# Kernel tuning notes

Hardware: AMD Instinct MI355X
Metric: run time of the kernel (lower is better)

The kernel has to match this reference:

```python
import jax, jax.numpy as jnp
import numpy as np

KLD_SCALE = 10.0
COMMIT_COST = 0.25


def setup_inputs() -> dict:
    key = jax.random.key(0)
    k1, k2, k3, k4 = jax.random.split(key, 4)
    B, C, T = 32, 512, 4096
    D, K = 128, 1024
    z = jax.random.normal(k1, (B, C, T), dtype=jnp.float32)
    proj_w = jax.random.normal(k2, (D, C), dtype=jnp.float32) * (1.0 / np.sqrt(C))
    proj_b = jax.random.normal(k3, (D,), dtype=jnp.float32) * 0.01
    embed_w = jax.random.normal(k4, (K, D), dtype=jnp.float32)
    return {"z": z, "proj_w": proj_w, "proj_b": proj_b, "embed_w": embed_w}


def reference(z, proj_w, proj_b, embed_w):
    B, C, T = z.shape
    D = proj_w.shape[0]
    # 1x1 Conv1d == per-timestep linear: [B,C,T] x [D,C] -> [B,T,D]
    z_e = jnp.einsum('bct,dc->btd', z, proj_w) + proj_b
    flat = z_e.reshape(-1, D)  # [B*T, D]
    # squared euclidean distances to codebook: [B*T, K]
    dist = (jnp.sum(flat * flat, axis=1, keepdims=True)
            - 2.0 * (flat @ embed_w.T)
            + jnp.sum(embed_w * embed_w, axis=1)[None, :])
    ind = jnp.argmin(dist, axis=1).reshape(B, T)  # == argmax(-dist)
    z_q = embed_w[ind]  # [B,T,D] codebook gather
    sg = jax.lax.stop_gradient
    diff = KLD_SCALE * (COMMIT_COST * jnp.mean((sg(z_q) - z_e) ** 2)
                        + jnp.mean((z_q - sg(z_e)) ** 2))
    z_q_ste = z_e + sg(z_q - z_e)  # straight-through estimator
    z_q_out = jnp.transpose(z_q_ste, (0, 2, 1))  # [B,D,T]
    return z_q_out, diff, ind
```

## Files before the change

kernel.cpp:

```cpp
#include <hip/hip_runtime.h>

#define B_N 32
#define C_N 512
#define T_N 4096
#define D_N 128
#define K_N 1024
#define N_N (B_N * T_N)

typedef _Float16 f16x8 __attribute__((ext_vector_type(8)));
typedef float    f32x4 __attribute__((ext_vector_type(4)));

#define ZSWZ_OFF 0
#define ESWZ_OFF 67108864
#define ENS_OFF  67895296
#define WSWZ_OFF 68431872
#define PART_OFF 68694016

#define GLL(g, s) __builtin_amdgcn_global_load_lds( \
    (const __attribute__((address_space(1))) unsigned int*)(g), \
    (__attribute__((address_space(3))) unsigned int*)(s), 16, 0, 0)

__global__ __launch_bounds__(128) void k_eprep(const float* __restrict__ E,
                                               _Float16* __restrict__ eswz,
                                               float* __restrict__ ens) {
  __shared__ float s2[2];
  const int code = blockIdx.x, d = threadIdx.x;
  const float e  = E[(size_t)code * D_N + d];
  const float es = e * 64.f;
  const _Float16 eh = (_Float16)es;
  const _Float16 el = (_Float16)(es - (float)eh);

  float sq = es * es;
  #pragma unroll
  for (int off = 32; off > 0; off >>= 1) sq += __shfl_down(sq, off);
  if ((d & 63) == 0) s2[d >> 6] = sq;
  __syncthreads();
  if (d == 0) ens[code] = s2[0] + s2[1];

  const int kt = code >> 7, mi = (code >> 4) & 7, lrow = code & 15;
  const int lk = (d >> 3) & 3, i = d & 7, cb = d >> 5;
  const size_t tile = (size_t)kt * 12;
  #define PUT(c, v) eswz[(((tile + (c)) * 512 + mi * 64 + lk * 16 + lrow) << 3) + i] = (v)
  PUT(cb, eh);
  PUT(4 + cb, el);
  PUT(8 + cb, eh);
  #undef PUT
}

__global__ __launch_bounds__(256) void k_wprep(const float* __restrict__ W,
                                               _Float16* __restrict__ wswz) {
  const int e = blockIdx.x * 256 + threadIdx.x;
  const int d = e >> 9, c = e & 511;
  const float x = W[d * C_N + c] * 8.f;
  const _Float16 h  = (_Float16)x;
  const _Float16 lo = (_Float16)(x - (float)h);
  const int kc = c >> 5, gg = (c >> 3) & 3, j = c & 7;
  const int nf = d >> 4, ll = gg * 16 + (d & 15);
  const size_t base = (size_t)kc * 8192 + ((size_t)nf * 64 + ll) * 8 + j;
  wswz[base]        = h;
  wswz[base + 4096] = lo;
}

__global__ __launch_bounds__(256, 2) void k_projm(const float* __restrict__ z,
                                                  const _Float16* __restrict__ wswz,
                                                  const float* __restrict__ bias,
                                                  f16x8* __restrict__ zswz) {
  __shared__ __align__(16) char lds[65536];

  const int tid = threadIdx.x;
  const int l   = tid & 63, w = tid >> 6;
  const int g   = l >> 4, li = l & 15;
  const int b   = blockIdx.y, t0 = blockIdx.x * 128;
  const float* zb = z + (size_t)b * C_N * T_N + t0;

  float bs[8];
  #pragma unroll
  for (int nf = 0; nf < 8; ++nf) bs[nf] = bias[nf * 16 + li] * 64.f;

  f32x4 acc[2][8];
  #pragma unroll
  for (int mi = 0; mi < 2; ++mi)
    #pragma unroll
    for (int nf = 0; nf < 8; ++nf) acc[mi][nf] = (f32x4)0.f;

  auto stage = [&](int kc, int buf) {
    char* zdst = lds + buf * 16384;
    char* wdst = lds + 32768 + buf * 16384;
    #pragma unroll
    for (int s = 0; s < 4; ++s) {
      const int q = w * 4 + s;
      const unsigned v = q * 64 + l;
      const unsigned u = v ^ (((v >> 8) & 1) << 2);
      GLL((const char*)zb +
              ((size_t)(kc * 32 + (u >> 5)) * T_N + (size_t)(u & 31) * 4) * 4,
          zdst + q * 1024);
      GLL((const char*)wswz + (size_t)kc * 16384 + q * 1024 + l * 16,
          wdst + q * 1024);
    }
  };

  stage(0, 0);
  __syncthreads();

  int buf = 0;
  for (int kc = 0; kc < 16; ++kc) {
    if (kc + 1 < 16) stage(kc + 1, buf ^ 1);

    const float* zl = (const float*)(lds + buf * 16384);
    const f16x8* wb = (const f16x8*)(lds + 32768 + buf * 16384);

    f16x8 ah[2], al[2];
    #pragma unroll
    for (int mi = 0; mi < 2; ++mi) {
      const int mt = w * 2 + mi;
      const int a0 = (g * 1024 + mt * 16 + li) ^ ((g & 1) << 4);
      #pragma unroll
      for (int j = 0; j < 8; ++j) {
        const float x = zl[a0 + j * 128] * 8.f;
        const _Float16 h = (_Float16)x;
        ah[mi][j] = h;
        al[mi][j] = (_Float16)(x - (float)h);
      }
    }
    f16x8 bh[8], bl[8];
    #pragma unroll
    for (int nf = 0; nf < 8; ++nf) {
      bh[nf] = wb[nf * 64 + l];
      bl[nf] = wb[512 + nf * 64 + l];
    }
    #pragma unroll
    for (int mi = 0; mi < 2; ++mi)
      #pragma unroll
      for (int nf = 0; nf < 8; ++nf) {
        acc[mi][nf] = __builtin_amdgcn_mfma_f32_16x16x32_f16(ah[mi], bh[nf], acc[mi][nf], 0, 0, 0);
        acc[mi][nf] = __builtin_amdgcn_mfma_f32_16x16x32_f16(al[mi], bh[nf], acc[mi][nf], 0, 0, 0);
        acc[mi][nf] = __builtin_amdgcn_mfma_f32_16x16x32_f16(ah[mi], bl[nf], acc[mi][nf], 0, 0, 0);
      }
    __syncthreads();
    buf ^= 1;
  }

  unsigned* cs = (unsigned*)lds;
  const int n0 = b * T_N + t0;
  for (int p = 0; p < 2; ++p) {
    #pragma unroll
    for (int mi = 0; mi < 2; ++mi) {
      const int trow = (w * 2 + mi) * 16 + g * 4;
      #pragma unroll
      for (int nfl = 0; nfl < 4; ++nfl) {
        const int nf = p * 4 + nfl;
        #pragma unroll
        for (int r = 0; r < 4; ++r) {
          const float x = acc[mi][nf][r] + bs[nf];
          const _Float16 h  = (_Float16)x;
          const _Float16 lo = (_Float16)(x - (float)h);
          cs[(trow + r) * 68 + nfl * 16 + li] =
              (unsigned)__builtin_bit_cast(unsigned short, h) |
              ((unsigned)__builtin_bit_cast(unsigned short, lo) << 16);
        }
      }
    }
    __syncthreads();
    #pragma unroll
    for (int i = 0; i < 4; ++i) {
      const int u = i * 256 + tid;
      const int t = u & 127, dc = u >> 7;
      f16x8 vh, vl;
      #pragma unroll
      for (int e = 0; e < 8; ++e) {
        const unsigned vv = cs[t * 68 + dc * 8 + e];
        vh[e] = __builtin_bit_cast(_Float16, (unsigned short)(vv & 0xffff));
        vl[e] = __builtin_bit_cast(_Float16, (unsigned short)(vv >> 16));
      }
      const int n = n0 + t;
      const int cu = p * 2 + (dc >> 2), lk = dc & 3;
      const size_t idx = ((size_t)(n >> 4) * 8 + cu) * 64 + lk * 16 + (n & 15);
      zswz[idx]       = vh;
      zswz[idx + 256] = vl;
    }
    __syncthreads();
  }
}

template<int NF0>
__device__ __forceinline__ float gather_reg(int wc, int l, const int* skf,
                                            const float* E, float* ob,
                                            const f16x8 (&bfr)[8][4]) {
  float psum = 0.f;
  #pragma unroll
  for (int nl = 0; nl < 2; ++nl) {
    constexpr int NFA[2] = {NF0, NF0 + 1};
    const int nf = NFA[nl];
    const int r = wc * 64 + nf * 16 + (l & 15);
    const int k = skf[r];
    const float* Er = E + (size_t)k * D_N;
    #pragma unroll
    for (int cu = 0; cu < 4; ++cu) {
      const int d0 = cu * 32 + (l >> 4) * 8;
      const float4 e0 = *(const float4*)(Er + d0);
      const float4 e1 = *(const float4*)(Er + d0 + 4);
      const float ev[8] = {e0.x, e0.y, e0.z, e0.w, e1.x, e1.y, e1.z, e1.w};
      const f16x8 hi = bfr[cu][nf];
      const f16x8 lo = bfr[cu + 4][nf];
      #pragma unroll
      for (int j = 0; j < 8; ++j) {
        const float ze = ((float)hi[j] + (float)lo[j]) * 0.015625f;
        const float df = ev[j] - ze;
        psum += df * df;
        ob[(size_t)(d0 + j) * T_N + r] = ev[j];
      }
    }
  }
  return psum;
}

__global__ __launch_bounds__(256, 2) void k_argmin5(const f16x8* __restrict__ zswz,
                                                    const f16x8* __restrict__ eswz,
                                                    const float* __restrict__ ens,
                                                    const float* __restrict__ E,
                                                    float* __restrict__ out,
                                                    float* __restrict__ indf,
                                                    float* __restrict__ part) {
  __shared__ __align__(16) char sbuf[65536];
  __shared__ float sdl[256];
  __shared__ int   skl[256];
  __shared__ int   skf[128];

  const int tid = threadIdx.x, l = tid & 63, w = tid >> 6;
  const int wr = w >> 1, wc = w & 1;
  const int blk = blockIdx.x;

  const char* zsrc = (const char*)zswz + (size_t)blk * 65536;
  #pragma unroll
  for (int s = 0; s < 16; ++s)
    GLL(zsrc + s * 4096 + tid * 16, sbuf + s * 4096 + w * 1024);
  asm volatile("s_waitcnt vmcnt(0)" ::: "memory");
  __syncthreads();

  f16x8 bfr[8][4];
  #pragma unroll
  for (int cu = 0; cu < 8; ++cu)
    #pragma unroll
    for (int nf = 0; nf < 4; ++nf)
      bfr[cu][nf] =
          *(const f16x8*)(sbuf + (((((wc * 4 + nf) * 8 + cu) * 64) + l) << 4));
  __syncthreads();

  const char* easrc = (const char*)eswz + (size_t)wr * 4096;

  float bestd[4];
  int   bestk[4];
  #pragma unroll
  for (int nf = 0; nf < 4; ++nf) { bestd[nf] = 3.4e38f; bestk[nf] = 0; }

  for (int kt = 0; kt < 8; ++kt) {
    f32x4 acc[4][4];
    #pragma unroll
    for (int mi = 0; mi < 4; ++mi)
      #pragma unroll
      for (int nf = 0; nf < 4; ++nf) acc[mi][nf] = (f32x4)0.f;

    #pragma unroll
    for (int c = 0; c < 12; ++c) {
      constexpr int CUMAP[12] = {0, 1, 2, 3, 0, 1, 2, 3, 4, 5, 6, 7};
      const int cu = CUMAP[c];
      f16x8 afr[4];
      #pragma unroll
      for (int mi = 0; mi < 4; ++mi)
        afr[mi] = *(const f16x8*)(easrc + (size_t)(kt * 12 + c) * 8192 +
                                  ((mi * 64 + l) << 4));
      #pragma unroll
      for (int mi = 0; mi < 4; ++mi)
        #pragma unroll
        for (int nf = 0; nf < 4; ++nf)
          acc[mi][nf] = __builtin_amdgcn_mfma_f32_16x16x32_f16(
              afr[mi], bfr[cu][nf], acc[mi][nf], 0, 0, 0);
    }

    #pragma unroll
    for (int mi = 0; mi < 4; ++mi) {
      const int cbase = kt * 128 + wr * 64 + mi * 16 + ((l >> 4) << 2);
      const float4 e4 = *(const float4*)&ens[cbase];
      const float ev[4] = {e4.x, e4.y, e4.z, e4.w};
      #pragma unroll
      for (int r = 0; r < 4; ++r) {
        const int k = cbase + r;
        #pragma unroll
        for (int nf = 0; nf < 4; ++nf) {
          const float dv = ev[r] - 2.0f * acc[mi][nf][r];
          if (dv < bestd[nf]) { bestd[nf] = dv; bestk[nf] = k; }
        }
      }
    }
  }

  #pragma unroll
  for (int nf = 0; nf < 4; ++nf) {
    float d = bestd[nf]; int k = bestk[nf];
    #pragma unroll
    for (int off = 16; off < 64; off <<= 1) {
      const float od = __shfl_xor(d, off);
      const int   ok = __shfl_xor(k, off);
      if (od < d || (od == d && ok < k)) { d = od; k = ok; }
    }
    if (l < 16) {
      sdl[wr * 128 + wc * 64 + nf * 16 + l] = d;
      skl[wr * 128 + wc * 64 + nf * 16 + l] = k;
    }
  }
  __syncthreads();
  if (tid < 128) {
    float d0 = sdl[tid], d1 = sdl[128 + tid];
    int   k0 = skl[tid], k1 = skl[128 + tid];
    if (d1 < d0 || (d1 == d0 && k1 < k0)) { d0 = d1; k0 = k1; }
    skf[tid] = k0;
    indf[blk * 128 + tid] = (float)k0;
  }
  __syncthreads();

  const int b  = blk >> 5;
  const int t0 = (blk & 31) << 7;
  float* ob = out + (size_t)b * (D_N * T_N) + t0;
  float psum = (wr == 0) ? gather_reg<0>(wc, l, skf, E, ob, bfr)
                         : gather_reg<2>(wc, l, skf, E, ob, bfr);
  #pragma unroll
  for (int off = 32; off > 0; off >>= 1) psum += __shfl_xor(psum, off);
  if (l == 0) part[blk * 4 + w] = psum;
}

__global__ __launch_bounds__(256) void k_diff(const float* __restrict__ part,
                                              float* __restrict__ diff_out) {
  __shared__ double wsd[4];
  const int tid = threadIdx.x;
  double s = 0.0;
  for (int i = tid; i < 4096; i += 256) s += (double)part[i];
  #pragma unroll
  for (int off = 32; off > 0; off >>= 1) s += __shfl_down(s, off);
  if ((tid & 63) == 0) wsd[tid >> 6] = s;
  __syncthreads();
  if (tid == 0) {
    const double tot = wsd[0] + wsd[1] + wsd[2] + wsd[3];
    diff_out[0] = (float)(12.5 * tot / (double)((size_t)N_N * D_N));
  }
}

extern "C" void kernel_launch(void* const* d_in, const int* in_sizes, int n_in,
                              void* d_out, int out_size, void* d_ws, size_t ws_size,
                              hipStream_t stream) {
  const float* z    = (const float*)d_in[0];
  const float* W    = (const float*)d_in[1];
  const float* bias = (const float*)d_in[2];
  const float* E    = (const float*)d_in[3];

  float* out = (float*)d_out;
  float* out_q    = out;
  float* out_diff = out + 16777216;
  float* out_ind  = out + 16777217;

  char* ws = (char*)d_ws;
  f16x8*    zswz = (f16x8*)(ws + ZSWZ_OFF);
  _Float16* eswz = (_Float16*)(ws + ESWZ_OFF);
  float*    ens  = (float*)(ws + ENS_OFF);
  _Float16* wswz = (_Float16*)(ws + WSWZ_OFF);
  float*    part = (float*)(ws + PART_OFF);

  k_eprep<<<K_N, 128, 0, stream>>>(E, eswz, ens);
  k_wprep<<<256, 256, 0, stream>>>(W, wswz);
  k_projm<<<dim3(T_N / 128, B_N), 256, 0, stream>>>(z, wswz, bias, zswz);
  k_argmin5<<<N_N / 128, 256, 0, stream>>>(zswz, (const f16x8*)eswz, ens, E,
                                           out_q, out_ind, part);
  k_diff<<<1, 256, 0, stream>>>(part, out_diff);
}
```

Measured before the change: 251.8 us.

## Halve argmin tile to 64 rows and double-buffer codebook through LDS

The argmin kernel now handles 64 timesteps per block instead of 128, which doubles the grid and halves the B-fragment registers each wave holds. Codebook fragments are no longer read straight from global memory by each wave. They are staged in a double-buffered LDS ring with async global-to-LDS loads, prefetching the next chunk while MFMAs run on the current one. The per-block partial sums are reduced in shared memory to one value per block. In exchange, the codebook is reloaded twice as many times overall and each chunk adds a barrier.

```diff
diff --git a/kernel.cpp b/kernel.cpp
--- a/kernel.cpp
+++ b/kernel.cpp
@@ -182,99 +182,88 @@
   }
 }
 
-template<int NF0>
-__device__ __forceinline__ float gather_reg(int wc, int l, const int* skf,
-                                            const float* E, float* ob,
-                                            const f16x8 (&bfr)[8][4]) {
-  float psum = 0.f;
-  #pragma unroll
-  for (int nl = 0; nl < 2; ++nl) {
-    constexpr int NFA[2] = {NF0, NF0 + 1};
-    const int nf = NFA[nl];
-    const int r = wc * 64 + nf * 16 + (l & 15);
-    const int k = skf[r];
-    const float* Er = E + (size_t)k * D_N;
-    #pragma unroll
-    for (int cu = 0; cu < 4; ++cu) {
-      const int d0 = cu * 32 + (l >> 4) * 8;
-      const float4 e0 = *(const float4*)(Er + d0);
-      const float4 e1 = *(const float4*)(Er + d0 + 4);
-      const float ev[8] = {e0.x, e0.y, e0.z, e0.w, e1.x, e1.y, e1.z, e1.w};
-      const f16x8 hi = bfr[cu][nf];
-      const f16x8 lo = bfr[cu + 4][nf];
-      #pragma unroll
-      for (int j = 0; j < 8; ++j) {
-        const float ze = ((float)hi[j] + (float)lo[j]) * 0.015625f;
-        const float df = ev[j] - ze;
-        psum += df * df;
-        ob[(size_t)(d0 + j) * T_N + r] = ev[j];
-      }
-    }
-  }
-  return psum;
-}
-
-__global__ __launch_bounds__(256, 2) void k_argmin5(const f16x8* __restrict__ zswz,
+__global__ __launch_bounds__(256, 2) void k_argmin6(const f16x8* __restrict__ zswz,
                                                     const f16x8* __restrict__ eswz,
                                                     const float* __restrict__ ens,
                                                     const float* __restrict__ E,
                                                     float* __restrict__ out,
                                                     float* __restrict__ indf,
                                                     float* __restrict__ part) {
-  __shared__ __align__(16) char sbuf[65536];
-  __shared__ float sdl[256];
-  __shared__ int   skl[256];
-  __shared__ int   skf[128];
+  __shared__ __align__(16) char sbuf[32768];
+  __shared__ float sdl[128];
+  __shared__ int   skl[128];
+  __shared__ int   skf[64];
+  __shared__ float wsum[4];
 
   const int tid = threadIdx.x, l = tid & 63, w = tid >> 6;
   const int wr = w >> 1, wc = w & 1;
   const int blk = blockIdx.x;
 
-  const char* zsrc = (const char*)zswz + (size_t)blk * 65536;
-  #pragma unroll
-  for (int s = 0; s < 16; ++s)
+  const char* zsrc = (const char*)zswz + (size_t)blk * 32768;
+  #pragma unroll
+  for (int s = 0; s < 8; ++s)
     GLL(zsrc + s * 4096 + tid * 16, sbuf + s * 4096 + w * 1024);
   asm volatile("s_waitcnt vmcnt(0)" ::: "memory");
   __syncthreads();
 
-  f16x8 bfr[8][4];
+  f16x8 bfr[8][2];
   #pragma unroll
   for (int cu = 0; cu < 8; ++cu)
     #pragma unroll
-    for (int nf = 0; nf < 4; ++nf)
+    for (int nf = 0; nf < 2; ++nf)
       bfr[cu][nf] =
-          *(const f16x8*)(sbuf + (((((wc * 4 + nf) * 8 + cu) * 64) + l) << 4));
-  __syncthreads();
-
-  const char* easrc = (const char*)eswz + (size_t)wr * 4096;
-
-  float bestd[4];
-  int   bestk[4];
-  #pragma unroll
-  for (int nf = 0; nf < 4; ++nf) { bestd[nf] = 3.4e38f; bestk[nf] = 0; }
+          *(const f16x8*)(sbuf + (((((wc * 2 + nf) * 8 + cu) * 64) + l) << 4));
+  __syncthreads();
+
+  const char* easrc = (const char*)eswz;
+  #pragma unroll
+  for (int s = 0; s < 4; ++s)
+    GLL(easrc + s * 4096 + tid * 16, sbuf + s * 4096 + w * 1024);
+
+  float bestd[2];
+  int   bestk[2];
+  #pragma unroll
+  for (int nf = 0; nf < 2; ++nf) { bestd[nf] = 3.4e38f; bestk[nf] = 0; }
 
   for (int kt = 0; kt < 8; ++kt) {
-    f32x4 acc[4][4];
+    f32x4 acc[4][2];
     #pragma unroll
     for (int mi = 0; mi < 4; ++mi)
       #pragma unroll
-      for (int nf = 0; nf < 4; ++nf) acc[mi][nf] = (f32x4)0.f;
-
-    #pragma unroll
-    for (int c = 0; c < 12; ++c) {
-      constexpr int CUMAP[12] = {0, 1, 2, 3, 0, 1, 2, 3, 4, 5, 6, 7};
-      const int cu = CUMAP[c];
-      f16x8 afr[4];
-      #pragma unroll
-      for (int mi = 0; mi < 4; ++mi)
-        afr[mi] = *(const f16x8*)(easrc + (size_t)(kt * 12 + c) * 8192 +
-                                  ((mi * 64 + l) << 4));
-      #pragma unroll
-      for (int mi = 0; mi < 4; ++mi)
-        #pragma unroll
-        for (int nf = 0; nf < 4; ++nf)
-          acc[mi][nf] = __builtin_amdgcn_mfma_f32_16x16x32_f16(
-              afr[mi], bfr[cu][nf], acc[mi][nf], 0, 0, 0);
+      for (int nf = 0; nf < 2; ++nf) acc[mi][nf] = (f32x4)0.f;
+
+    #pragma unroll
+    for (int pp = 0; pp < 6; ++pp) {
+      const int p = kt * 6 + pp;
+      char* rbuf  = sbuf + (size_t)(p & 1) * 16384;
+      char* wbufp = sbuf + (size_t)((p + 1) & 1) * 16384;
+
+      __syncthreads();
+
+      if (p + 1 < 48) {
+        const size_t nb = (size_t)(p + 1) * 16384;
+        #pragma unroll
+        for (int s = 0; s < 4; ++s)
+          GLL(easrc + nb + s * 4096 + tid * 16, wbufp + s * 4096 + w * 1024);
+      }
+
+      #pragma unroll
+      for (int j = 0; j < 2; ++j) {
+        constexpr int CUMAP[12] = {0, 1, 2, 3, 0, 1, 2, 3, 4, 5, 6, 7};
+        const int c  = pp * 2 + j;
+        const int cu = CUMAP[c];
+        f16x8 afr[4];
+        #pragma unroll
+        for (int mi = 0; mi < 4; ++mi)
+          afr[mi] = *(const f16x8*)(rbuf + (size_t)j * 8192 +
+                                    (((wr * 4 + mi) * 64 + l) << 4));
+        #pragma unroll
+        for (int mi = 0; mi < 4; ++mi)
+          #pragma unroll
+          for (int nf = 0; nf < 2; ++nf)
+            acc[mi][nf] = __builtin_amdgcn_mfma_f32_16x16x32_f16(
+                afr[mi], bfr[cu][nf], acc[mi][nf], 0, 0, 0);
+      }
     }
 
     #pragma unroll
@@ -286,7 +275,7 @@
       for (int r = 0; r < 4; ++r) {
         const int k = cbase + r;
         #pragma unroll
-        for (int nf = 0; nf < 4; ++nf) {
+        for (int nf = 0; nf < 2; ++nf) {
           const float dv = ev[r] - 2.0f * acc[mi][nf][r];
           if (dv < bestd[nf]) { bestd[nf] = dv; bestk[nf] = k; }
         }
@@ -295,7 +284,7 @@
   }
 
   #pragma unroll
-  for (int nf = 0; nf < 4; ++nf) {
+  for (int nf = 0; nf < 2; ++nf) {
     float d = bestd[nf]; int k = bestk[nf];
     #pragma unroll
     for (int off = 16; off < 64; off <<= 1) {
@@ -304,28 +293,50 @@
       if (od < d || (od == d && ok < k)) { d = od; k = ok; }
     }
     if (l < 16) {
-      sdl[wr * 128 + wc * 64 + nf * 16 + l] = d;
-      skl[wr * 128 + wc * 64 + nf * 16 + l] = k;
-    }
-  }
-  __syncthreads();
-  if (tid < 128) {
-    float d0 = sdl[tid], d1 = sdl[128 + tid];
-    int   k0 = skl[tid], k1 = skl[128 + tid];
+      sdl[wr * 64 + wc * 32 + nf * 16 + l] = d;
+      skl[wr * 64 + wc * 32 + nf * 16 + l] = k;
+    }
+  }
+  __syncthreads();
+  if (tid < 64) {
+    float d0 = sdl[tid], d1 = sdl[64 + tid];
+    int   k0 = skl[tid], k1 = skl[64 + tid];
     if (d1 < d0 || (d1 == d0 && k1 < k0)) { d0 = d1; k0 = k1; }
     skf[tid] = k0;
-    indf[blk * 128 + tid] = (float)k0;
-  }
-  __syncthreads();
-
-  const int b  = blk >> 5;
-  const int t0 = (blk & 31) << 7;
+    indf[blk * 64 + tid] = (float)k0;
+  }
+  __syncthreads();
+
+  const int b  = blk >> 6;
+  const int t0 = (blk & 63) << 6;
   float* ob = out + (size_t)b * (D_N * T_N) + t0;
-  float psum = (wr == 0) ? gather_reg<0>(wc, l, skf, E, ob, bfr)
-                         : gather_reg<2>(wc, l, skf, E, ob, bfr);
+  float psum = 0.f;
+  {
+    const int r = wc * 32 + wr * 16 + (l & 15);
+    const int k = skf[r];
+    const float* Er = E + (size_t)k * D_N;
+    #pragma unroll
+    for (int cu = 0; cu < 4; ++cu) {
+      const int d0 = cu * 32 + (l >> 4) * 8;
+      const float4 e0 = *(const float4*)(Er + d0);
+      const float4 e1 = *(const float4*)(Er + d0 + 4);
+      const float ev[8] = {e0.x, e0.y, e0.z, e0.w, e1.x, e1.y, e1.z, e1.w};
+      const f16x8 hi = bfr[cu][wr];
+      const f16x8 lo = bfr[cu + 4][wr];
+      #pragma unroll
+      for (int j = 0; j < 8; ++j) {
+        const float ze = ((float)hi[j] + (float)lo[j]) * 0.015625f;
+        const float df = ev[j] - ze;
+        psum += df * df;
+        ob[(size_t)(d0 + j) * T_N + r] = ev[j];
+      }
+    }
+  }
   #pragma unroll
   for (int off = 32; off > 0; off >>= 1) psum += __shfl_xor(psum, off);
-  if (l == 0) part[blk * 4 + w] = psum;
+  if (l == 0) wsum[w] = psum;
+  __syncthreads();
+  if (tid == 0) part[blk] = wsum[0] + wsum[1] + wsum[2] + wsum[3];
 }
 
 __global__ __launch_bounds__(256) void k_diff(const float* __restrict__ part,
@@ -333,7 +344,7 @@
   __shared__ double wsd[4];
   const int tid = threadIdx.x;
   double s = 0.0;
-  for (int i = tid; i < 4096; i += 256) s += (double)part[i];
+  for (int i = tid; i < 2048; i += 256) s += (double)part[i];
   #pragma unroll
   for (int off = 32; off > 0; off >>= 1) s += __shfl_down(s, off);
   if ((tid & 63) == 0) wsd[tid >> 6] = s;
@@ -367,7 +378,7 @@
   k_eprep<<<K_N, 128, 0, stream>>>(E, eswz, ens);
   k_wprep<<<256, 256, 0, stream>>>(W, wswz);
   k_projm<<<dim3(T_N / 128, B_N), 256, 0, stream>>>(z, wswz, bias, zswz);
-  k_argmin5<<<N_N / 128, 256, 0, stream>>>(zswz, (const f16x8*)eswz, ens, E,
-                                           out_q, out_ind, part);
+  k_argmin6<<<N_N / 64, 256, 0, stream>>>(zswz, (const f16x8*)eswz, ens, E,
+                                          out_q, out_ind, part);
   k_diff<<<1, 256, 0, stream>>>(part, out_diff);
 }
```

New measurement: 251.3 us. No clear change (-0.2%).
